# Performance work log

Hardware: AMD Instinct MI355X
Metric: run time of the kernel (lower is better)

## Reference

```python
import jax, jax.numpy as jnp
import numpy as np

TAU = 2.0        # LIF membrane time constant
VTH = 0.5        # spike threshold
EPS = 1e-5       # BatchNorm eps
ALPHA = 2.0      # ATan surrogate alpha (spikingjelly default)


@jax.custom_vjp
def atan_heaviside(x):
    # forward: Heaviside spike; backward: ATan surrogate gradient
    return (x >= 0.0).astype(x.dtype)

def _ah_fwd(x):
    return atan_heaviside(x), x

def _ah_bwd(x, g):
    return (g * (ALPHA / 2.0) / (1.0 + (jnp.pi / 2.0 * ALPHA * x) ** 2),)

atan_heaviside.defvjp(_ah_fwd, _ah_bwd)


def lif_multistep(x):
    # x: [T, ...] -> spikes [T, ...]; hard reset to 0, decay_input=True
    def step(v, xt):
        v = v + (xt - v) / TAU
        s = atan_heaviside(v - VTH)
        v = v * (1.0 - jax.lax.stop_gradient(s))  # detach_reset=True
        return v, s
    v0 = jnp.zeros_like(x[0])
    _, spikes = jax.lax.scan(step, v0, x)
    return spikes


def tape_pe(d_model, max_len, dtype):
    # tAPE (ConvTran): sinusoidal PE with d_model/max_len frequency scaling
    pos = jnp.arange(max_len, dtype=dtype)[:, None]
    div = jnp.exp(jnp.arange(0, d_model, 2, dtype=dtype) * (-np.log(10000.0) / d_model))
    arg = pos * div * (d_model / max_len)
    pe = jnp.zeros((max_len, d_model), dtype)
    pe = pe.at[:, 0::2].set(jnp.sin(arg))
    pe = pe.at[:, 1::2].set(jnp.cos(arg))
    return pe  # [N, D]


def setup_inputs() -> dict:
    key = jax.random.key(0)
    k1, k2 = jax.random.split(key)
    T, B, N, P, D = 4, 64, 196, 768, 256
    x = jax.random.normal(k1, (T, B, N, P), dtype=jnp.float32)
    W = jax.random.normal(k2, (D, P), dtype=jnp.float32) * 0.02
    gamma = jnp.ones((D,), dtype=jnp.float32)
    beta = jnp.zeros((D,), dtype=jnp.float32)
    return {"x": x, "W": W, "gamma": gamma, "beta": beta}


def reference(x, W, gamma, beta):
    T, B, N, P = x.shape
    D = W.shape[0]
    # patch linear (no bias): [T,B,N,P] @ [D,P]^T -> [T,B,N,D]
    h = jnp.einsum('tbnp,dp->tbnd', x, W)
    h = jnp.transpose(h, (0, 1, 3, 2))  # [T,B,D,N]
    # BatchNorm1d over channel D (training-mode batch stats over T*B and N)
    mean = h.mean(axis=(0, 1, 3), keepdims=True)
    var = ((h - mean) ** 2).mean(axis=(0, 1, 3), keepdims=True)
    h = (h - mean) * jax.lax.rsqrt(var + EPS)
    h = h * gamma[None, None, :, None] + beta[None, None, :, None]
    # LIF spiking neuron scan over T
    h = lif_multistep(h)
    # tAPE positional encoding (broadcast [D,N] over T,B) + second LIF
    h = h + tape_pe(D, N, h.dtype).T
    h = lif_multistep(h)
    return jnp.transpose(h, (0, 1, 3, 2))  # [T,B,N,D]
```

## Files before the change

### kernel.cpp

```cpp
#include <hip/hip_runtime.h>
#include <cmath>

#define T_    4
#define B_    64
#define N_    196
#define P_    768
#define D_    256
#define BN_   (B_*N_)
#define M_    (T_*BN_)
#define SITES (BN_*D_)

#define TILE  64
#define TK    16
#define KITER (P_/TK)
#define MBLKS (M_/TILE)
#define NBLKS (D_/TILE)
#define RLEN  98

typedef __attribute__((ext_vector_type(2))) float f32x2;

__device__ __forceinline__ void pk_fma(f32x2& acc, f32x2 a, f32x2 b) {
    f32x2 t;
    asm("v_pk_mul_f32 %1, %2, %3\n\t"
        "v_pk_add_f32 %0, %0, %1"
        : "+v"(acc), "=&v"(t) : "v"(a), "v"(b));
}

extern "C" __global__ __launch_bounds__(256)
void gemm_f32emu(const float* __restrict__ x, const float* __restrict__ w,
                 float* __restrict__ h, float* __restrict__ hT) {
    __shared__ __align__(16) f32x2 As2[2][TK/2][RLEN];
    __shared__ __align__(16) f32x2 Bs2[2][TK/2][RLEN];

    const int tid  = threadIdx.x;
    const int tx   = tid & 15;
    const int ty   = tid >> 4;
    const int bid  = blockIdx.x;
    const int xcd  = bid & 7;
    const int lin  = bid >> 3;
    const int m0   = (xcd * 98 + (lin >> 2)) * TILE;
    const int d0   = (lin & 3) * TILE;
    const int lrow = tid >> 2;
    const int kq   = tid & 3;
    const int lk   = kq * 4;
    const int woff = (lrow >> 2) * 6 + (lrow & 3);
    const int abase = ty * 6;
    const int bbase = tx * 6;

    const float* xp = x + (size_t)(m0 + lrow) * P_ + lk;
    const float* wp = w + (size_t)(d0 + lrow) * P_ + lk;

    f32x2 acc[4][4][2];
#pragma unroll
    for (int i = 0; i < 4; ++i)
#pragma unroll
        for (int j = 0; j < 4; ++j)
#pragma unroll
            for (int p = 0; p < 2; ++p) acc[i][j][p] = f32x2{0.0f, 0.0f};

    {
        const float4 av = *(const float4*)xp;
        const float4 bv = *(const float4*)wp;
        As2[0][kq * 2 + 0][woff] = f32x2{av.x, av.y};
        As2[0][kq * 2 + 1][woff] = f32x2{av.z, av.w};
        Bs2[0][kq * 2 + 0][woff] = f32x2{bv.x, bv.y};
        Bs2[0][kq * 2 + 1][woff] = f32x2{bv.z, bv.w};
    }

    int cur = 0;
    for (int k0 = 0; k0 < KITER; ++k0) {
        __syncthreads();
        float4 av, bv;
        const bool have = (k0 + 1 < KITER);
        if (have) {
            av = *(const float4*)(xp + (k0 + 1) * TK);
            bv = *(const float4*)(wp + (k0 + 1) * TK);
        }
#pragma unroll
        for (int kp = 0; kp < TK / 2; ++kp) {
            const int pi = kp & 1;
            const f32x2* Ar = As2[cur][kp];
            const f32x2* Br = Bs2[cur][kp];
            const float4 aa0 = *(const float4*)(Ar + abase);
            const float4 aa1 = *(const float4*)(Ar + abase + 2);
            const float4 bb0 = *(const float4*)(Br + bbase);
            const float4 bb1 = *(const float4*)(Br + bbase + 2);
            f32x2 a2[4], b2[4];
            a2[0] = f32x2{aa0.x, aa0.y}; a2[1] = f32x2{aa0.z, aa0.w};
            a2[2] = f32x2{aa1.x, aa1.y}; a2[3] = f32x2{aa1.z, aa1.w};
            b2[0] = f32x2{bb0.x, bb0.y}; b2[1] = f32x2{bb0.z, bb0.w};
            b2[2] = f32x2{bb1.x, bb1.y}; b2[3] = f32x2{bb1.z, bb1.w};
#pragma unroll
            for (int i = 0; i < 4; ++i)
#pragma unroll
                for (int j = 0; j < 4; ++j)
                    pk_fma(acc[i][j][pi], a2[i], b2[j]);
        }
        if (have) {
            As2[cur ^ 1][kq * 2 + 0][woff] = f32x2{av.x, av.y};
            As2[cur ^ 1][kq * 2 + 1][woff] = f32x2{av.z, av.w};
            Bs2[cur ^ 1][kq * 2 + 0][woff] = f32x2{bv.x, bv.y};
            Bs2[cur ^ 1][kq * 2 + 1][woff] = f32x2{bv.z, bv.w};
        }
        cur ^= 1;
    }

    float res[4][4];
#pragma unroll
    for (int i = 0; i < 4; ++i)
#pragma unroll
        for (int j = 0; j < 4; ++j) {
            const float l01 = __fadd_rn(acc[i][j][0].x, acc[i][j][0].y);
            const float l23 = __fadd_rn(acc[i][j][1].x, acc[i][j][1].y);
            res[i][j] = __fadd_rn(l01, l23);
        }
#pragma unroll
    for (int i = 0; i < 4; ++i) {
        float4 o = {res[i][0], res[i][1], res[i][2], res[i][3]};
        *(float4*)(h + (size_t)(m0 + ty * 4 + i) * D_ + d0 + tx * 4) = o;
    }
    if (hT) {
#pragma unroll
        for (int j = 0; j < 4; ++j) {
            float4 o = {res[0][j], res[1][j], res[2][j], res[3][j]};
            *(float4*)(hT + (size_t)(d0 + tx * 4 + j) * M_ + m0 + ty * 4) = o;
        }
    }
}

#define MCH2 7168
#define GRP  224
extern "C" __global__ __launch_bounds__(256)
void mean_hT(const float* __restrict__ hT, float* __restrict__ mean_) {
    __shared__ float buf[2][MCH2];
    const int tid = threadIdx.x;
    const float* src = hT + (size_t)blockIdx.x * M_;

#pragma unroll
    for (int u = 0; u < 7; ++u)
        *(float4*)&buf[0][(u * 256 + tid) * 4] =
            *(const float4*)&src[(u * 256 + tid) * 4];
    __syncthreads();

    float acc = 0.0f;
    for (int c = 0; c < 7; ++c) {
        const int cb = c & 1;
        const bool have = (c + 1 < 7);
        float4 v[7];
        if (have) {
            const float* rp = src + (c + 1) * MCH2;
#pragma unroll
            for (int u = 0; u < 7; ++u)
                v[u] = *(const float4*)&rp[(u * 256 + tid) * 4];
        }
        if (tid == 0) {
            const float4* bp = (const float4*)buf[cb];
            float4 p0[8], p1[8];
#pragma unroll
            for (int u = 0; u < 8; ++u) p0[u] = bp[u];
            for (int gp = 0; gp < GRP; gp += 2) {
#pragma unroll
                for (int u = 0; u < 8; ++u) p1[u] = bp[(gp + 1) * 8 + u];
#pragma unroll
                for (int u = 0; u < 8; ++u) {
                    acc = __fadd_rn(acc, p0[u].x);
                    acc = __fadd_rn(acc, p0[u].y);
                    acc = __fadd_rn(acc, p0[u].z);
                    acc = __fadd_rn(acc, p0[u].w);
                }
                const int g2 = (gp + 2 < GRP) ? gp + 2 : 0;
#pragma unroll
                for (int u = 0; u < 8; ++u) p0[u] = bp[g2 * 8 + u];
#pragma unroll
                for (int u = 0; u < 8; ++u) {
                    acc = __fadd_rn(acc, p1[u].x);
                    acc = __fadd_rn(acc, p1[u].y);
                    acc = __fadd_rn(acc, p1[u].z);
                    acc = __fadd_rn(acc, p1[u].w);
                }
            }
        }
        if (have) {
#pragma unroll
            for (int u = 0; u < 7; ++u)
                *(float4*)&buf[cb ^ 1][(u * 256 + tid) * 4] = v[u];
        }
        __syncthreads();
    }
    if (tid == 0) mean_[blockIdx.x] = __fdiv_rn(acc, 50176.0f);
}

extern "C" __global__ __launch_bounds__(256)
void var_hT(const float* __restrict__ hT, const float* __restrict__ mean_,
            float* __restrict__ inv_) {
    __shared__ float chunks[256];
    const int d    = blockIdx.x;
    const int tid  = threadIdx.x;
    const int wv   = tid >> 6;
    const int lane = tid & 63;
    const float mn = mean_[d];
    const float* col = hT + (size_t)d * M_;

    for (int tb = wv; tb < T_ * B_; tb += 4) {
        double part = 0.0;
        for (int n = lane; n < N_; n += 64) {
            const float hv = col[tb * N_ + n];
            const float t1 = __fsub_rn(hv, mn);
            const float sq = __fmul_rn(t1, t1);
            part += (double)sq;
        }
#pragma unroll
        for (int off = 32; off; off >>= 1) part += __shfl_down(part, off);
        if (lane == 0) chunks[tb] = (float)part;
    }
    __syncthreads();
    if (tid == 0) {
        float accf = 0.0f;
        for (int tb = 0; tb < T_ * B_; ++tb) accf = __fadd_rn(accf, chunks[tb]);
        const float var = __fdiv_rn(accf, 50176.0f);
        inv_[d] = __fdiv_rn(1.0f, __fsqrt_rn(__fadd_rn(var, 1e-5f)));
    }
}

#define MCH  256
#define DCH  16
#define PADW 20
#define NCHK (M_/MCH)

extern "C" __global__ __launch_bounds__(256)
void mean_seq(const float* __restrict__ h, float* __restrict__ mean_) {
    __shared__ __align__(16) float buf[2][MCH][PADW];
    const int tid = threadIdx.x;
    const int d0  = blockIdx.x * DCH;
    {
        const float* rp = h + (size_t)tid * D_ + d0;
        *(float4*)&buf[0][tid][0]  = *(const float4*)(rp + 0);
        *(float4*)&buf[0][tid][4]  = *(const float4*)(rp + 4);
        *(float4*)&buf[0][tid][8]  = *(const float4*)(rp + 8);
        *(float4*)&buf[0][tid][12] = *(const float4*)(rp + 12);
    }
    __syncthreads();
    float acc = 0.0f;
    for (int c = 0; c < NCHK; ++c) {
        const int cb = c & 1;
        const bool have = (c + 1 < NCHK);
        float4 v0, v1, v2, v3;
        if (have) {
            const float* rp = h + ((size_t)(c + 1) * MCH + tid) * D_ + d0;
            v0 = *(const float4*)(rp + 0);
            v1 = *(const float4*)(rp + 4);
            v2 = *(const float4*)(rp + 8);
            v3 = *(const float4*)(rp + 12);
        }
        if (tid < DCH) {
#pragma unroll 16
            for (int m = 0; m < MCH; ++m)
                acc = __fadd_rn(acc, buf[cb][m][tid]);
        }
        if (have) {
            *(float4*)&buf[cb ^ 1][tid][0]  = v0;
            *(float4*)&buf[cb ^ 1][tid][4]  = v1;
            *(float4*)&buf[cb ^ 1][tid][8]  = v2;
            *(float4*)&buf[cb ^ 1][tid][12] = v3;
        }
        __syncthreads();
    }
    if (tid < DCH) mean_[d0 + tid] = __fdiv_rn(acc, 50176.0f);
}

extern "C" __global__ __launch_bounds__(64)
void var_seq(const float* __restrict__ h, const float* __restrict__ mean_,
             float* __restrict__ inv_) {
    const int d    = blockIdx.x;
    const int lane = threadIdx.x;
    const float mn = mean_[d];
    float accf = 0.0f;
    for (int tb = 0; tb < T_ * B_; ++tb) {
        double part = 0.0;
        for (int n = lane; n < N_; n += 64) {
            const float hv = h[((size_t)tb * N_ + n) * D_ + d];
            const float t1 = __fsub_rn(hv, mn);
            const float sq = __fmul_rn(t1, t1);
            part += (double)sq;
        }
#pragma unroll
        for (int off = 32; off; off >>= 1) part += __shfl_down(part, off);
        accf = __fadd_rn(accf, (float)part);
    }
    if (lane == 0) {
        const float var = __fdiv_rn(accf, 50176.0f);
        inv_[d] = __fdiv_rn(1.0f, __fsqrt_rn(__fadd_rn(var, 1e-5f)));
    }
}

extern "C" __global__ __launch_bounds__(256)
void pe_build(float* __restrict__ pe_) {
    const int d = threadIdx.x;
    const int n = blockIdx.x;
    const double dv  = exp((double)(d & ~1) * (-9.210340371976184 / 256.0));
    const double arg = ((double)n * dv) * (256.0 / 196.0);
    pe_[(size_t)n * D_ + d] = (d & 1) ? (float)cos(arg) : (float)sin(arg);
}

extern "C" __global__ __launch_bounds__(256)
void lif_final(float* __restrict__ out, const float* __restrict__ mean_,
               const float* __restrict__ inv_, const float* __restrict__ gamma,
               const float* __restrict__ beta, const float* __restrict__ pe_tab) {
    const int idx = blockIdx.x * 256 + threadIdx.x;
    const int d = idx & (D_ - 1);
    const int n = (idx >> 8) % N_;

    const float mn = mean_[d];
    const float iv = inv_[d];
    const float g  = gamma[d];
    const float b  = beta[d];

    float pe;
    if (pe_tab) {
        pe = pe_tab[(size_t)n * D_ + d];
    } else {
        const double dv  = exp((double)(d & ~1) * (-9.210340371976184 / 256.0));
        const double arg = ((double)n * dv) * (256.0 / 196.0);
        pe = (d & 1) ? (float)cos(arg) : (float)sin(arg);
    }

    float hv[4];
#pragma unroll
    for (int t = 0; t < T_; ++t) hv[t] = out[(size_t)t * SITES + idx];

    float v1 = 0.0f, v2 = 0.0f, s2v[4];
#pragma unroll
    for (int t = 0; t < T_; ++t) {
        const float t1 = __fsub_rn(hv[t], mn);
        const float u  = __fmul_rn(t1, iv);
        const float hb = __fadd_rn(__fmul_rn(u, g), b);
        v1 = __fadd_rn(v1, __fmul_rn(__fsub_rn(hb, v1), 0.5f));
        const float s1 = (v1 >= 0.5f) ? 1.0f : 0.0f;
        v1 = __fmul_rn(v1, __fsub_rn(1.0f, s1));
        const float y = __fadd_rn(s1, pe);
        v2 = __fadd_rn(v2, __fmul_rn(__fsub_rn(y, v2), 0.5f));
        const float s2 = (v2 >= 0.5f) ? 1.0f : 0.0f;
        v2 = __fmul_rn(v2, __fsub_rn(1.0f, s2));
        s2v[t] = s2;
    }
#pragma unroll
    for (int t = 0; t < T_; ++t) out[(size_t)t * SITES + idx] = s2v[t];
}

extern "C" void kernel_launch(void* const* d_in, const int* in_sizes, int n_in,
                              void* d_out, int out_size, void* d_ws, size_t ws_size,
                              hipStream_t stream) {
    const float* x     = (const float*)d_in[0];
    const float* w     = (const float*)d_in[1];
    const float* gamma = (const float*)d_in[2];
    const float* beta  = (const float*)d_in[3];
    float* out = (float*)d_out;

    float* mean_ = (float*)d_ws;
    float* inv_  = mean_ + D_;
    float* pe_   = inv_  + D_;
    float* hT_   = pe_   + (size_t)N_ * D_;

    const size_t need_pe = (size_t)(2 * D_ + N_ * D_) * sizeof(float);
    const size_t need_hT = need_pe + (size_t)M_ * D_ * sizeof(float);
    const bool use_pe = ws_size >= need_pe;
    const bool use_hT = ws_size >= need_hT;

    gemm_f32emu<<<MBLKS * NBLKS, 256, 0, stream>>>(x, w, out,
                                                   use_hT ? hT_ : nullptr);
    if (use_hT) {
        mean_hT<<<D_, 256, 0, stream>>>(hT_, mean_);
        var_hT<<<D_, 256, 0, stream>>>(hT_, mean_, inv_);
    } else {
        mean_seq<<<16, 256, 0, stream>>>(out, mean_);
        var_seq<<<D_, 64, 0, stream>>>(out, mean_, inv_);
    }
    if (use_pe) pe_build<<<N_, 256, 0, stream>>>(pe_);
    lif_final<<<SITES / 256, 256, 0, stream>>>(out, mean_, inv_, gamma, beta,
                                               use_pe ? pe_ : nullptr);
}
```

Before: 855.6 us.

## Enlarge GEMM tile to 128x64 and fuse mean/variance kernels

The GEMM block tile grows from 64x64 to 128x64, with each thread computing an 8x4 micro-tile instead of 4x4. This raises arithmetic intensity per shared-memory load and halves the grid size, at the cost of more accumulator registers and possibly lower occupancy. Separately, the mean and variance kernels over the transposed activations are merged into one kernel, which saves a launch and lets the variance pass reuse the column while it may still be in cache.

```diff
diff --git a/kernel.cpp b/kernel.cpp
--- a/kernel.cpp
+++ b/kernel.cpp
@@ -10,12 +10,13 @@
 #define M_    (T_*BN_)
 #define SITES (BN_*D_)
 
-#define TILE  64
+#define BM    128
+#define BN2   64
 #define TK    16
 #define KITER (P_/TK)
-#define MBLKS (M_/TILE)
-#define NBLKS (D_/TILE)
-#define RLEN  98
+#define GBLKS ((M_/BM)*(D_/BN2))
+#define ALEN  194
+#define BLEN  98
 
 typedef __attribute__((ext_vector_type(2))) float f32x2;
 
@@ -29,85 +30,97 @@
 extern "C" __global__ __launch_bounds__(256)
 void gemm_f32emu(const float* __restrict__ x, const float* __restrict__ w,
                  float* __restrict__ h, float* __restrict__ hT) {
-    __shared__ __align__(16) f32x2 As2[2][TK/2][RLEN];
-    __shared__ __align__(16) f32x2 Bs2[2][TK/2][RLEN];
-
-    const int tid  = threadIdx.x;
-    const int tx   = tid & 15;
-    const int ty   = tid >> 4;
-    const int bid  = blockIdx.x;
-    const int xcd  = bid & 7;
-    const int lin  = bid >> 3;
-    const int m0   = (xcd * 98 + (lin >> 2)) * TILE;
-    const int d0   = (lin & 3) * TILE;
-    const int lrow = tid >> 2;
-    const int kq   = tid & 3;
-    const int lk   = kq * 4;
-    const int woff = (lrow >> 2) * 6 + (lrow & 3);
-    const int abase = ty * 6;
-    const int bbase = tx * 6;
-
-    const float* xp = x + (size_t)(m0 + lrow) * P_ + lk;
-    const float* wp = w + (size_t)(d0 + lrow) * P_ + lk;
-
-    f32x2 acc[4][4][2];
-#pragma unroll
-    for (int i = 0; i < 4; ++i)
+    __shared__ __align__(16) f32x2 As2[2][TK/2][ALEN];
+    __shared__ __align__(16) f32x2 Bs2[2][TK/2][BLEN];
+
+    const int tid = threadIdx.x;
+    const int tx  = tid & 15;
+    const int ty  = tid >> 4;
+    const int bid = blockIdx.x;
+    const int xcd = bid & 7;
+    const int lin = bid >> 3;
+    const int m0  = (xcd * 49 + (lin >> 2)) * BM;
+    const int d0  = (lin & 3) * BN2;
+
+    const int ar = tid >> 1;
+    const int sa = (tid & 1) * 8;
+    const int ra = (tid & 1) * 4;
+    const int ga = (ar >> 2) * 6 + (ar & 3);
+    const int br = tid >> 2;
+    const int qb = tid & 3;
+    const int gb = (br >> 2) * 6 + (br & 3);
+
+    const float* xp = x + (size_t)(m0 + ar) * P_ + sa;
+    const float* wp = w + (size_t)(d0 + br) * P_ + qb * 4;
+
+    f32x2 acc[8][4][2];
+#pragma unroll
+    for (int i = 0; i < 8; ++i)
 #pragma unroll
         for (int j = 0; j < 4; ++j)
 #pragma unroll
             for (int p = 0; p < 2; ++p) acc[i][j][p] = f32x2{0.0f, 0.0f};
 
     {
-        const float4 av = *(const float4*)xp;
-        const float4 bv = *(const float4*)wp;
-        As2[0][kq * 2 + 0][woff] = f32x2{av.x, av.y};
-        As2[0][kq * 2 + 1][woff] = f32x2{av.z, av.w};
-        Bs2[0][kq * 2 + 0][woff] = f32x2{bv.x, bv.y};
-        Bs2[0][kq * 2 + 1][woff] = f32x2{bv.z, bv.w};
+        const float4 va0 = *(const float4*)(xp);
+        const float4 va1 = *(const float4*)(xp + 4);
+        const float4 vb  = *(const float4*)(wp);
+        As2[0][ra + 0][ga] = f32x2{va0.x, va0.y};
+        As2[0][ra + 1][ga] = f32x2{va0.z, va0.w};
+        As2[0][ra + 2][ga] = f32x2{va1.x, va1.y};
+        As2[0][ra + 3][ga] = f32x2{va1.z, va1.w};
+        Bs2[0][qb * 2 + 0][gb] = f32x2{vb.x, vb.y};
+        Bs2[0][qb * 2 + 1][gb] = f32x2{vb.z, vb.w};
     }
 
     int cur = 0;
     for (int k0 = 0; k0 < KITER; ++k0) {
         __syncthreads();
-        float4 av, bv;
+        float4 va0, va1, vb;
         const bool have = (k0 + 1 < KITER);
         if (have) {
-            av = *(const float4*)(xp + (k0 + 1) * TK);
-            bv = *(const float4*)(wp + (k0 + 1) * TK);
+            va0 = *(const float4*)(xp + (k0 + 1) * TK);
+            va1 = *(const float4*)(xp + (k0 + 1) * TK + 4);
+            vb  = *(const float4*)(wp + (k0 + 1) * TK);
         }
 #pragma unroll
         for (int kp = 0; kp < TK / 2; ++kp) {
             const int pi = kp & 1;
             const f32x2* Ar = As2[cur][kp];
             const f32x2* Br = Bs2[cur][kp];
-            const float4 aa0 = *(const float4*)(Ar + abase);
-            const float4 aa1 = *(const float4*)(Ar + abase + 2);
-            const float4 bb0 = *(const float4*)(Br + bbase);
-            const float4 bb1 = *(const float4*)(Br + bbase + 2);
-            f32x2 a2[4], b2[4];
-            a2[0] = f32x2{aa0.x, aa0.y}; a2[1] = f32x2{aa0.z, aa0.w};
-            a2[2] = f32x2{aa1.x, aa1.y}; a2[3] = f32x2{aa1.z, aa1.w};
-            b2[0] = f32x2{bb0.x, bb0.y}; b2[1] = f32x2{bb0.z, bb0.w};
-            b2[2] = f32x2{bb1.x, bb1.y}; b2[3] = f32x2{bb1.z, bb1.w};
-#pragma unroll
-            for (int i = 0; i < 4; ++i)
+            const float4 A0 = *(const float4*)(Ar + ty * 12);
+            const float4 A1 = *(const float4*)(Ar + ty * 12 + 2);
+            const float4 A2 = *(const float4*)(Ar + ty * 12 + 6);
+            const float4 A3 = *(const float4*)(Ar + ty * 12 + 8);
+            const float4 B0 = *(const float4*)(Br + tx * 6);
+            const float4 B1 = *(const float4*)(Br + tx * 6 + 2);
+            f32x2 af[8], bf[4];
+            af[0] = f32x2{A0.x, A0.y}; af[1] = f32x2{A0.z, A0.w};
+            af[2] = f32x2{A1.x, A1.y}; af[3] = f32x2{A1.z, A1.w};
+            af[4] = f32x2{A2.x, A2.y}; af[5] = f32x2{A2.z, A2.w};
+            af[6] = f32x2{A3.x, A3.y}; af[7] = f32x2{A3.z, A3.w};
+            bf[0] = f32x2{B0.x, B0.y}; bf[1] = f32x2{B0.z, B0.w};
+            bf[2] = f32x2{B1.x, B1.y}; bf[3] = f32x2{B1.z, B1.w};
+#pragma unroll
+            for (int i = 0; i < 8; ++i)
 #pragma unroll
                 for (int j = 0; j < 4; ++j)
-                    pk_fma(acc[i][j][pi], a2[i], b2[j]);
-        }
-        if (have) {
-            As2[cur ^ 1][kq * 2 + 0][woff] = f32x2{av.x, av.y};
-            As2[cur ^ 1][kq * 2 + 1][woff] = f32x2{av.z, av.w};
-            Bs2[cur ^ 1][kq * 2 + 0][woff] = f32x2{bv.x, bv.y};
-            Bs2[cur ^ 1][kq * 2 + 1][woff] = f32x2{bv.z, bv.w};
+                    pk_fma(acc[i][j][pi], af[i], bf[j]);
+        }
+        if (have) {
+            As2[cur ^ 1][ra + 0][ga] = f32x2{va0.x, va0.y};
+            As2[cur ^ 1][ra + 1][ga] = f32x2{va0.z, va0.w};
+            As2[cur ^ 1][ra + 2][ga] = f32x2{va1.x, va1.y};
+            As2[cur ^ 1][ra + 3][ga] = f32x2{va1.z, va1.w};
+            Bs2[cur ^ 1][qb * 2 + 0][gb] = f32x2{vb.x, vb.y};
+            Bs2[cur ^ 1][qb * 2 + 1][gb] = f32x2{vb.z, vb.w};
         }
         cur ^= 1;
     }
 
-    float res[4][4];
-#pragma unroll
-    for (int i = 0; i < 4; ++i)
+    float res[8][4];
+#pragma unroll
+    for (int i = 0; i < 8; ++i)
 #pragma unroll
         for (int j = 0; j < 4; ++j) {
             const float l01 = __fadd_rn(acc[i][j][0].x, acc[i][j][0].y);
@@ -115,15 +128,18 @@
             res[i][j] = __fadd_rn(l01, l23);
         }
 #pragma unroll
-    for (int i = 0; i < 4; ++i) {
+    for (int i = 0; i < 8; ++i) {
         float4 o = {res[i][0], res[i][1], res[i][2], res[i][3]};
-        *(float4*)(h + (size_t)(m0 + ty * 4 + i) * D_ + d0 + tx * 4) = o;
+        *(float4*)(h + (size_t)(m0 + ty * 8 + i) * D_ + d0 + tx * 4) = o;
     }
     if (hT) {
 #pragma unroll
         for (int j = 0; j < 4; ++j) {
-            float4 o = {res[0][j], res[1][j], res[2][j], res[3][j]};
-            *(float4*)(hT + (size_t)(d0 + tx * 4 + j) * M_ + m0 + ty * 4) = o;
+            float4 o0 = {res[0][j], res[1][j], res[2][j], res[3][j]};
+            float4 o1 = {res[4][j], res[5][j], res[6][j], res[7][j]};
+            float* col = hT + (size_t)(d0 + tx * 4 + j) * M_ + m0 + ty * 8;
+            *(float4*)(col)     = o0;
+            *(float4*)(col + 4) = o1;
         }
     }
 }
@@ -131,10 +147,14 @@
 #define MCH2 7168
 #define GRP  224
 extern "C" __global__ __launch_bounds__(256)
-void mean_hT(const float* __restrict__ hT, float* __restrict__ mean_) {
+void meanvar_hT(const float* __restrict__ hT, float* __restrict__ mean_,
+                float* __restrict__ inv_) {
     __shared__ float buf[2][MCH2];
+    __shared__ float chunks[256];
+    __shared__ float mn_sh;
     const int tid = threadIdx.x;
-    const float* src = hT + (size_t)blockIdx.x * M_;
+    const int d   = blockIdx.x;
+    const float* src = hT + (size_t)d * M_;
 
 #pragma unroll
     for (int u = 0; u < 7; ++u)
@@ -187,24 +207,20 @@
         }
         __syncthreads();
     }
-    if (tid == 0) mean_[blockIdx.x] = __fdiv_rn(acc, 50176.0f);
-}
-
-extern "C" __global__ __launch_bounds__(256)
-void var_hT(const float* __restrict__ hT, const float* __restrict__ mean_,
-            float* __restrict__ inv_) {
-    __shared__ float chunks[256];
-    const int d    = blockIdx.x;
-    const int tid  = threadIdx.x;
+    if (tid == 0) {
+        const float mn = __fdiv_rn(acc, 50176.0f);
+        mean_[d] = mn;
+        mn_sh = mn;
+    }
+    __syncthreads();
+
+    const float mn = mn_sh;
     const int wv   = tid >> 6;
     const int lane = tid & 63;
-    const float mn = mean_[d];
-    const float* col = hT + (size_t)d * M_;
-
     for (int tb = wv; tb < T_ * B_; tb += 4) {
         double part = 0.0;
         for (int n = lane; n < N_; n += 64) {
-            const float hv = col[tb * N_ + n];
+            const float hv = src[tb * N_ + n];
             const float t1 = __fsub_rn(hv, mn);
             const float sq = __fmul_rn(t1, t1);
             part += (double)sq;
@@ -366,11 +382,9 @@
     const bool use_pe = ws_size >= need_pe;
     const bool use_hT = ws_size >= need_hT;
 
-    gemm_f32emu<<<MBLKS * NBLKS, 256, 0, stream>>>(x, w, out,
-                                                   use_hT ? hT_ : nullptr);
+    gemm_f32emu<<<GBLKS, 256, 0, stream>>>(x, w, out, use_hT ? hT_ : nullptr);
     if (use_hT) {
-        mean_hT<<<D_, 256, 0, stream>>>(hT_, mean_);
-        var_hT<<<D_, 256, 0, stream>>>(hT_, mean_, inv_);
+        meanvar_hT<<<D_, 256, 0, stream>>>(hT_, mean_, inv_);
     } else {
         mean_seq<<<16, 256, 0, stream>>>(out, mean_);
         var_seq<<<D_, 64, 0, stream>>>(out, mean_, inv_);
```

New measurement: 866.0 us. About the same (+1.2%).
